# Performance work log

Hardware: AMD Instinct MI355X
Metric: run time of the kernel (lower is better)

The kernel has to match this reference:

```python
import jax, jax.numpy as jnp
import numpy as np

B = 8192          # tokens
H = 7168          # hidden size
E = 256           # routed experts
N_GROUP = 8
GROUP_SIZE = 32   # E // N_GROUP
TOPK_GROUP = 4
TOPK = 8
SCALE = 2.5
EPS = 1e-20
NEG_INF = -jnp.inf


def setup_inputs() -> dict:
    key = jax.random.key(0)
    k1, k2, k3 = jax.random.split(key, 3)
    x = jax.random.normal(k1, (1, 1, B, H), dtype=jnp.float32)
    weight = jax.random.normal(k2, (H, E), dtype=jnp.float32) * 0.02
    bias = jax.random.uniform(k3, (E,), dtype=jnp.float32)  # e_score_correction_bias
    return {"x": x, "weight": weight, "bias": bias}


def reference(x, weight, bias):
    # gate projection + softmax over experts
    logits = jnp.einsum('abth,he->abte', x, weight)          # [1,1,B,E]
    scores = jax.nn.softmax(logits, axis=-1)                 # [1,1,B,E]
    scores_with_bias = scores + bias                         # bias-corrected scores

    # group-limited routing: top-2 per group, summed -> group score
    grouped = scores_with_bias.reshape(1, 1, B, N_GROUP, GROUP_SIZE)
    top2_vals, _ = jax.lax.top_k(grouped, 2)                 # [1,1,B,8,2]
    group_scores = top2_vals.sum(axis=-1)                    # [1,1,B,8]

    # select top-4 groups, build {1, -inf} mask over groups
    _, top4_idx = jax.lax.top_k(group_scores, TOPK_GROUP)    # [1,1,B,4]
    sel = jax.nn.one_hot(top4_idx, N_GROUP, dtype=scores.dtype).sum(axis=-2)  # [1,1,B,8]
    group_mask = jnp.where(sel > 0, 1.0, NEG_INF)
    expert_mask = jnp.repeat(group_mask, GROUP_SIZE, axis=-1)  # [1,1,B,256]

    # mask (multiplicative, as in original), top-8 experts
    masked = scores_with_bias * expert_mask
    _, top8_idx = jax.lax.top_k(masked, TOPK)                # [1,1,B,8]

    # gather unbiased scores, normalize, eps + scale
    w = jnp.take_along_axis(scores, top8_idx, axis=-1)       # [1,1,B,8]
    w = w / w.sum(axis=-1, keepdims=True)
    w = (w + EPS) * SCALE
    return w, top8_idx
```

## Files before the change

kernel.cpp:

```cpp
#include <hip/hip_runtime.h>
#include <math.h>

#define B_TOK 8192
#define H_DIM 7168
#define E_NUM 256
#define NKS   8
#define KSL   (H_DIM / NKS)
#define BK    32
#define NSTEP (KSL / BK)
#define BM    128
#define NMT   (B_TOK / BM)
#define FLAG_CAP 512
#define TAU   2e-6

typedef _Float16 f16;
typedef __attribute__((ext_vector_type(8))) _Float16 f16x8;
typedef __attribute__((ext_vector_type(4))) float    f32x4;

typedef __attribute__((address_space(1))) const void gvoid_t;
typedef __attribute__((address_space(3))) void       lvoid_t;

__device__ inline void gload_lds16(const void* g, void* s) {
    __builtin_amdgcn_global_load_lds((gvoid_t*)g, (lvoid_t*)s, 16, 0, 0);
}

__device__ __forceinline__ void route_token(
    const double* lv, const double* bj, int l, int hf, int t,
    float* __restrict__ out, double* ming_adj, double* ming_grp)
{
    double m = fmax(fmax(lv[0], lv[1]), fmax(lv[2], lv[3]));
    #pragma unroll
    for (int d = 1; d < 64; d <<= 1) m = fmax(m, __shfl_xor(m, d, 64));
    double sc[4], zs = 0.0;
    #pragma unroll
    for (int q = 0; q < 4; ++q) { sc[q] = exp(lv[q] - m); zs += sc[q]; }
    #pragma unroll
    for (int d = 1; d < 64; d <<= 1) zs += __shfl_xor(zs, d, 64);
    double swb[4];
    #pragma unroll
    for (int q = 0; q < 4; ++q) { sc[q] /= zs; swb[q] = sc[q] + bj[q]; }

    double gsq[4];
    #pragma unroll
    for (int q = 0; q < 4; ++q) {
        double a = swb[q], b = -INFINITY;
        #pragma unroll
        for (int d = 1; d <= 16; d <<= 1) {
            double oa = __shfl_xor(a, d, 64), ob = __shfl_xor(b, d, 64);
            double na = fmax(a, oa);
            double nb = fmax(fmin(a, oa), fmax(b, ob));
            a = na; b = nb;
        }
        gsq[q] = a + b;
    }
    double gsv[8];
    #pragma unroll
    for (int q = 0; q < 4; ++q) {
        gsv[2 * q]     = __shfl(gsq[q], 0, 64);
        gsv[2 * q + 1] = __shfl(gsq[q], 32, 64);
    }

    unsigned selmask = 0; double g4 = 0.0, g5 = 0.0;
    #pragma unroll
    for (int k = 0; k < 5; ++k) {
        double best = -INFINITY; int bg = 0;
        #pragma unroll
        for (int g = 0; g < 8; ++g)
            if (gsv[g] > best) { best = gsv[g]; bg = g; }
        if (k < 4) { selmask |= 1u << bg; g4 = best; } else g5 = best;
        #pragma unroll
        for (int g = 0; g < 8; ++g) if (g == bg) gsv[g] = -INFINITY;
    }
    *ming_grp = g4 - g5;

    double mk[4];
    #pragma unroll
    for (int q = 0; q < 4; ++q)
        mk[q] = ((selmask >> (2 * q + hf)) & 1u) ? swb[q] : -INFINITY;

    double wk[8]; int ek[8]; double wsum = 0.0;
    double prev = 0.0, ming = 1e300;
    #pragma unroll
    for (int k = 0; k < 9; ++k) {
        double vbest = mk[0]; int ebest = l;
        #pragma unroll
        for (int q = 1; q < 4; ++q)
            if (mk[q] > vbest) { vbest = mk[q]; ebest = l + 64 * q; }
        #pragma unroll
        for (int d = 1; d < 64; d <<= 1) {
            double ov = __shfl_xor(vbest, d, 64);
            int    oe = __shfl_xor(ebest, d, 64);
            if (ov > vbest || (ov == vbest && oe < ebest)) { vbest = ov; ebest = oe; }
        }
        if (k > 0) ming = fmin(ming, prev - vbest);
        prev = vbest;
        if (k < 8) {
            const int ol = ebest & 63, oq = ebest >> 6;
            if (l == ol) {
                #pragma unroll
                for (int q = 0; q < 4; ++q) if (q == oq) mk[q] = -INFINITY;
            }
            double cand = (oq == 0) ? sc[0] : (oq == 1) ? sc[1] : (oq == 2) ? sc[2] : sc[3];
            double sv = __shfl(cand, ol, 64);
            wk[k] = sv; ek[k] = ebest; wsum += sv;
        }
    }
    *ming_adj = ming;

    if (l == 0) {
        const double inv = 1.0 / wsum;
        #pragma unroll
        for (int k = 0; k < 8; ++k) {
            out[(size_t)t * 8 + k] = (float)((wk[k] * inv + 1e-20) * 2.5);
            out[(size_t)B_TOK * 8 + (size_t)t * 8 + k] = (float)ek[k];
        }
    }
}

__global__ void convert_w_kernel(const float* __restrict__ W,
                                 f16* __restrict__ wpk,
                                 unsigned* __restrict__ flags) {
    if (blockIdx.x == 0 && threadIdx.x == 0) flags[0] = 0;
    int g = blockIdx.x * 256 + threadIdx.x;
    int n = g & 255, k = g >> 8;
    float v = W[(size_t)k * E_NUM + n];
    f16 hi = (f16)v;
    f16 lo = (f16)(v - (float)hi);
    int kf = k >> 5, tq = (k >> 3) & 3, j = k & 7;
    int nf = n >> 4, l = tq * 16 + (n & 15);
    size_t off = ((size_t)(kf * 32 + nf * 2)) * 512 + (size_t)l * 8 + j;
    wpk[off]       = hi;
    wpk[off + 512] = lo;
}

__device__ __forceinline__ void stage_B(const f16* __restrict__ wb, int kf,
                                        char* lds, int wid, int l) {
    #pragma unroll
    for (int i = 0; i < 4; ++i) {
        int fi = wid * 4 + i;
        gload_lds16(wb + ((size_t)kf * 32 + fi) * 512 + (size_t)l * 8,
                    lds + 16384 + fi * 1024);
    }
}

__device__ __forceinline__ void write_A(char* lds, int wid, int l,
                                        float4 a0, float4 a1) {
    float fv[8] = {a0.x, a0.y, a0.z, a0.w, a1.x, a1.y, a1.z, a1.w};
    f16x8 hv, lo;
    #pragma unroll
    for (int j = 0; j < 8; ++j) {
        f16 hh = (f16)fv[j];
        hv[j] = hh;
        lo[j] = (f16)(fv[j] - (float)hh);
    }
    *reinterpret_cast<f16x8*>(&lds[(wid * 2 + 0) * 1024 + l * 16]) = hv;
    *reinterpret_cast<f16x8*>(&lds[(wid * 2 + 1) * 1024 + l * 16]) = lo;
}

__device__ __forceinline__ void compute_step(const char* lds, int wr, int wc,
                                             int l, f32x4 (&acc)[4][4]) {
    const char* Ab = lds;
    const char* Bb = lds + 16384;
    f16x8 af[4][2], bf[4][2];
    #pragma unroll
    for (int mi = 0; mi < 4; ++mi)
        #pragma unroll
        for (int h = 0; h < 2; ++h)
            af[mi][h] = *reinterpret_cast<const f16x8*>(
                Ab + ((wr * 4 + mi) * 2 + h) * 1024 + l * 16);
    #pragma unroll
    for (int ni = 0; ni < 4; ++ni)
        #pragma unroll
        for (int h = 0; h < 2; ++h)
            bf[ni][h] = *reinterpret_cast<const f16x8*>(
                Bb + ((wc * 4 + ni) * 2 + h) * 1024 + l * 16);
    #pragma unroll
    for (int mi = 0; mi < 4; ++mi)
        #pragma unroll
        for (int ni = 0; ni < 4; ++ni) {
            acc[mi][ni] = __builtin_amdgcn_mfma_f32_16x16x32_f16(
                af[mi][0], bf[ni][0], acc[mi][ni], 0, 0, 0);
            acc[mi][ni] = __builtin_amdgcn_mfma_f32_16x16x32_f16(
                af[mi][0], bf[ni][1], acc[mi][ni], 0, 0, 0);
            acc[mi][ni] = __builtin_amdgcn_mfma_f32_16x16x32_f16(
                af[mi][1], bf[ni][0], acc[mi][ni], 0, 0, 0);
        }
}

__global__ __launch_bounds__(512, 4)
void gemm_kernel(const float* __restrict__ x,
                 const f16* __restrict__ wpk,
                 float* __restrict__ partial) {
    __shared__ __align__(16) char lds[49152];

    const int tid = threadIdx.x;
    const int l   = tid & 63;
    const int wid = tid >> 6;
    const int bid = blockIdx.x;
    const int ks  = bid & 7;
    const int mt  = bid >> 3;
    const int wr  = wid >> 2;
    const int wc  = wid & 3;

    const int row = mt * BM + wid * 16 + (l & 15);
    const float* xrow = x + (size_t)row * H_DIM + ks * KSL + (l >> 4) * 8;
    const f16* wb = wpk + (size_t)ks * NSTEP * 32 * 512;

    f32x4 acc[4][4];
    #pragma unroll
    for (int mi = 0; mi < 4; ++mi)
        #pragma unroll
        for (int ni = 0; ni < 4; ++ni) acc[mi][ni] = (f32x4)0.0f;

    float4 a0 = *reinterpret_cast<const float4*>(xrow);
    float4 a1 = *reinterpret_cast<const float4*>(xrow + 4);
    stage_B(wb, 0, lds, wid, l);
    write_A(lds, wid, l, a0, a1);
    a0 = *reinterpret_cast<const float4*>(xrow + BK);
    a1 = *reinterpret_cast<const float4*>(xrow + BK + 4);
    __syncthreads();

    for (int t = 0; t < NSTEP; ++t) {
        float4 a0n, a1n;
        if (t + 2 < NSTEP) {
            a0n = *reinterpret_cast<const float4*>(xrow + (size_t)(t + 2) * BK);
            a1n = *reinterpret_cast<const float4*>(xrow + (size_t)(t + 2) * BK + 4);
        }
        compute_step(lds, wr, wc, l, acc);
        __syncthreads();
        if (t + 1 < NSTEP) {
            stage_B(wb, t + 1, lds, wid, l);
            write_A(lds, wid, l, a0, a1);
            a0 = a0n; a1 = a1n;
            __syncthreads();
        }
    }

    float* pbase = partial + ((size_t)ks * B_TOK + (size_t)mt * BM) * E_NUM;
    #pragma unroll
    for (int mi = 0; mi < 4; ++mi)
        #pragma unroll
        for (int ni = 0; ni < 4; ++ni)
            #pragma unroll
            for (int r = 0; r < 4; ++r) {
                int rr = wr * 64 + mi * 16 + (l >> 4) * 4 + r;
                int cc = wc * 64 + ni * 16 + (l & 15);
                pbase[(size_t)rr * E_NUM + cc] = acc[mi][ni][r];
            }
}

__global__ __launch_bounds__(512, 1)
void routing_kernel(const float* __restrict__ partial,
                    const float* __restrict__ bias,
                    float* __restrict__ out,
                    unsigned* __restrict__ flags) {
    const int tid  = threadIdx.x;
    const int l    = tid & 63;
    const int wv   = tid >> 6;
    const int tok0 = blockIdx.x * 32;

    double bj[4];
    #pragma unroll
    for (int q = 0; q < 4; ++q) bj[q] = (double)bias[l + 64 * q];
    const int hf = l >> 5;

    for (int i = 0; i < 4; ++i) {
        const int t = tok0 + wv * 4 + i;
        double lv[4];
        #pragma unroll
        for (int q = 0; q < 4; ++q) {
            double s = 0.0;
            #pragma unroll
            for (int ksl = 0; ksl < NKS; ++ksl)
                s += (double)partial[((size_t)ksl * B_TOK + t) * E_NUM + l + 64 * q];
            lv[q] = s;
        }
        double ma, mg;
        route_token(lv, bj, l, hf, t, out, &ma, &mg);
        if (l == 0 && (ma < TAU || mg < TAU)) {
            unsigned idx = atomicAdd(&flags[0], 1u);
            if (idx < FLAG_CAP) flags[1 + idx] = (unsigned)t;
        }
    }
}

__global__ __launch_bounds__(256)
void recompute_dot_kernel(const float* __restrict__ x,
                          const float* __restrict__ W,
                          const unsigned* __restrict__ flags,
                          double* __restrict__ dpart) {
    __shared__ float xs[896];
    unsigned count = flags[0]; if (count > FLAG_CAP) count = FLAG_CAP;
    unsigned nj = count * 8;
    for (unsigned j = blockIdx.x; j < nj; j += gridDim.x) {
        unsigned li = j >> 3, sl = j & 7;
        int t = (int)flags[1 + li];
        const float* xb = x + (size_t)t * H_DIM + sl * 896;
        for (int i = threadIdx.x; i < 224; i += 256)
            *reinterpret_cast<float4*>(&xs[i * 4]) =
                *reinterpret_cast<const float4*>(xb + i * 4);
        __syncthreads();
        const float* wp = W + (size_t)(sl * 896) * E_NUM + threadIdx.x;
        double acc = 0.0;
        #pragma unroll 8
        for (int k = 0; k < 896; ++k)
            acc += (double)xs[k] * (double)wp[(size_t)k * E_NUM];
        dpart[((size_t)li * 8 + sl) * E_NUM + threadIdx.x] = acc;
        __syncthreads();
    }
}

__global__ __launch_bounds__(64)
void recompute_route_kernel(const double* __restrict__ dpart,
                            const float* __restrict__ bias,
                            const unsigned* __restrict__ flags,
                            float* __restrict__ out) {
    const int l = threadIdx.x;
    unsigned count = flags[0]; if (count > FLAG_CAP) count = FLAG_CAP;
    double bj[4];
    #pragma unroll
    for (int q = 0; q < 4; ++q) bj[q] = (double)bias[l + 64 * q];
    const int hf = l >> 5;
    for (unsigned li = blockIdx.x; li < count; li += gridDim.x) {
        int t = (int)flags[1 + li];
        double lv[4];
        #pragma unroll
        for (int q = 0; q < 4; ++q) {
            double s = 0.0;
            #pragma unroll
            for (int sl = 0; sl < 8; ++sl)
                s += dpart[((size_t)li * 8 + sl) * E_NUM + l + 64 * q];
            lv[q] = s;
        }
        double ma, mg;
        route_token(lv, bj, l, hf, t, out, &ma, &mg);
    }
}

#define TM 32
#define HB 64
#define FNST (H_DIM / HB)

__global__ __launch_bounds__(512, 1)
void moe_gate_fallback(const float* __restrict__ x,
                       const float* __restrict__ W,
                       const float* __restrict__ bias,
                       float* __restrict__ out) {
    __shared__ double xs[TM][HB];
    const int tid  = threadIdx.x;
    const int l    = tid & 63;
    const int wv   = tid >> 6;
    const int tok0 = blockIdx.x * TM;
    const int tl = tid >> 4;
    const int ho = (tid & 15) * 4;

    double acc[4][4];
    #pragma unroll
    for (int i = 0; i < 4; ++i)
        #pragma unroll
        for (int q = 0; q < 4; ++q) acc[i][q] = 0.0;

    const float* xrow = x + (size_t)(tok0 + tl) * H_DIM + ho;
    float4 v = *reinterpret_cast<const float4*>(xrow);

    for (int s = 0; s < FNST; ++s) {
        __syncthreads();
        xs[tl][ho + 0] = (double)v.x;
        xs[tl][ho + 1] = (double)v.y;
        xs[tl][ho + 2] = (double)v.z;
        xs[tl][ho + 3] = (double)v.w;
        __syncthreads();
        const int sn = (s + 1 < FNST) ? s + 1 : s;
        v = *reinterpret_cast<const float4*>(xrow + (size_t)sn * HB);
        const float* wh = W + (size_t)s * HB * E_NUM + l;
        #pragma unroll 4
        for (int h = 0; h < HB; h += 2) {
            float wf0[4], wf1[4];
            #pragma unroll
            for (int q = 0; q < 4; ++q) {
                wf0[q] = wh[(size_t)h       * E_NUM + q * 64];
                wf1[q] = wh[(size_t)(h + 1) * E_NUM + q * 64];
            }
            #pragma unroll
            for (int i = 0; i < 4; ++i) {
                const double2 xv = *reinterpret_cast<const double2*>(&xs[wv * 4 + i][h]);
                #pragma unroll
                for (int q = 0; q < 4; ++q) {
                    acc[i][q] = fma((double)wf0[q], xv.x, acc[i][q]);
                    acc[i][q] = fma((double)wf1[q], xv.y, acc[i][q]);
                }
            }
        }
    }

    double bj[4];
    #pragma unroll
    for (int q = 0; q < 4; ++q) bj[q] = (double)bias[l + 64 * q];
    const int hf = l >> 5;

    for (int i = 0; i < 4; ++i) {
        const int t = tok0 + wv * 4 + i;
        double lv[4];
        #pragma unroll
        for (int q = 0; q < 4; ++q) lv[q] = acc[i][q];
        double ma, mg;
        route_token(lv, bj, l, hf, t, out, &ma, &mg);
    }
}

extern "C" void kernel_launch(void* const* d_in, const int* in_sizes, int n_in,
                              void* d_out, int out_size, void* d_ws, size_t ws_size,
                              hipStream_t stream) {
    const float* x    = (const float*)d_in[0];
    const float* W    = (const float*)d_in[1];
    const float* bias = (const float*)d_in[2];
    float* out = (float*)d_out;

    const size_t flag_off = 7864320;
    const size_t part_off = 8u * 1024 * 1024;
    const size_t need     = part_off + (size_t)NKS * B_TOK * E_NUM * 4;

    if (ws_size >= need) {
        f16*      wpk     = (f16*)d_ws;
        unsigned* flags   = (unsigned*)((char*)d_ws + flag_off);
        float*    partial = (float*)((char*)d_ws + part_off);
        double*   dpart   = (double*)((char*)d_ws + part_off);

        convert_w_kernel<<<(H_DIM * E_NUM) / 256, 256, 0, stream>>>(W, wpk, flags);
        gemm_kernel<<<NMT * NKS, 512, 0, stream>>>(x, wpk, partial);
        routing_kernel<<<B_TOK / 32, 512, 0, stream>>>(partial, bias, out, flags);
        recompute_dot_kernel<<<1024, 256, 0, stream>>>(x, W, flags, dpart);
        recompute_route_kernel<<<64, 64, 0, stream>>>(dpart, bias, flags, out);
    } else {
        moe_gate_fallback<<<B_TOK / 32, 512, 0, stream>>>(x, W, bias, out);
    }
}
```

Baseline: 236.6 us.

## Retile GEMM to 64-row blocks, vectorize weight conversion, add MFMA priority

The GEMM tile drops from 128 to 64 rows, and blocks go from 512 to 256 threads. Each wave now covers all 64 rows and its own 64-column slice, which changes the A/B staging and LDS layout. The weight conversion kernel now has each thread write 8 packed halves as vector stores instead of scattered scalar stores. The MFMA loop is wrapped in s_setprio, and the recompute_dot launch size is halved. Together these target the conversion's store cost and GEMM occupancy and scheduling, at the cost of more redundant B loads per token.

New measurement: 231.0 us. -2.4%, faster.

```diff
diff --git a/kernel.cpp b/kernel.cpp
--- a/kernel.cpp
+++ b/kernel.cpp
@@ -8,7 +8,7 @@
 #define KSL   (H_DIM / NKS)
 #define BK    32
 #define NSTEP (KSL / BK)
-#define BM    128
+#define BM    64
 #define NMT   (B_TOK / BM)
 #define FLAG_CAP 512
 #define TAU   2e-6
@@ -121,30 +121,39 @@
                                  f16* __restrict__ wpk,
                                  unsigned* __restrict__ flags) {
     if (blockIdx.x == 0 && threadIdx.x == 0) flags[0] = 0;
-    int g = blockIdx.x * 256 + threadIdx.x;
-    int n = g & 255, k = g >> 8;
-    float v = W[(size_t)k * E_NUM + n];
-    f16 hi = (f16)v;
-    f16 lo = (f16)(v - (float)hi);
-    int kf = k >> 5, tq = (k >> 3) & 3, j = k & 7;
-    int nf = n >> 4, l = tq * 16 + (n & 15);
-    size_t off = ((size_t)(kf * 32 + nf * 2)) * 512 + (size_t)l * 8 + j;
-    wpk[off]       = hi;
-    wpk[off + 512] = lo;
+    int gid = blockIdx.x * 256 + threadIdx.x;
+    int fgp = gid >> 6;
+    int l   = gid & 63;
+    int kf = fgp >> 4, nf = fgp & 15;
+    int rb  = kf * 32 + (l >> 4) * 8;
+    int col = nf * 16 + (l & 15);
+    f16x8 hv, lv;
+    #pragma unroll
+    for (int j = 0; j < 8; ++j) {
+        float v = W[(size_t)(rb + j) * E_NUM + col];
+        f16 hh = (f16)v;
+        hv[j] = hh;
+        lv[j] = (f16)(v - (float)hh);
+    }
+    *reinterpret_cast<f16x8*>(&wpk[(size_t)fgp * 1024 + l * 8])       = hv;
+    *reinterpret_cast<f16x8*>(&wpk[(size_t)fgp * 1024 + 512 + l * 8]) = lv;
 }
 
 __device__ __forceinline__ void stage_B(const f16* __restrict__ wb, int kf,
                                         char* lds, int wid, int l) {
     #pragma unroll
-    for (int i = 0; i < 4; ++i) {
-        int fi = wid * 4 + i;
+    for (int i = 0; i < 8; ++i) {
+        int fi = wid * 8 + i;
         gload_lds16(wb + ((size_t)kf * 32 + fi) * 512 + (size_t)l * 8,
-                    lds + 16384 + fi * 1024);
-    }
-}
-
-__device__ __forceinline__ void write_A(char* lds, int wid, int l,
+                    lds + 8192 + fi * 1024);
+    }
+}
+
+__device__ __forceinline__ void write_A(char* lds, int tid,
                                         float4 a0, float4 a1) {
+    const int r  = tid >> 2;
+    const int mf = r >> 4;
+    const int l  = (tid & 3) * 16 + (r & 15);
     float fv[8] = {a0.x, a0.y, a0.z, a0.w, a1.x, a1.y, a1.z, a1.w};
     f16x8 hv, lo;
     #pragma unroll
@@ -153,27 +162,28 @@
         hv[j] = hh;
         lo[j] = (f16)(fv[j] - (float)hh);
     }
-    *reinterpret_cast<f16x8*>(&lds[(wid * 2 + 0) * 1024 + l * 16]) = hv;
-    *reinterpret_cast<f16x8*>(&lds[(wid * 2 + 1) * 1024 + l * 16]) = lo;
-}
-
-__device__ __forceinline__ void compute_step(const char* lds, int wr, int wc,
-                                             int l, f32x4 (&acc)[4][4]) {
+    *reinterpret_cast<f16x8*>(&lds[(mf * 2 + 0) * 1024 + l * 16]) = hv;
+    *reinterpret_cast<f16x8*>(&lds[(mf * 2 + 1) * 1024 + l * 16]) = lo;
+}
+
+__device__ __forceinline__ void compute_step(const char* lds, int wc, int l,
+                                             f32x4 (&acc)[4][4]) {
     const char* Ab = lds;
-    const char* Bb = lds + 16384;
+    const char* Bb = lds + 8192;
     f16x8 af[4][2], bf[4][2];
     #pragma unroll
     for (int mi = 0; mi < 4; ++mi)
         #pragma unroll
         for (int h = 0; h < 2; ++h)
             af[mi][h] = *reinterpret_cast<const f16x8*>(
-                Ab + ((wr * 4 + mi) * 2 + h) * 1024 + l * 16);
+                Ab + (mi * 2 + h) * 1024 + l * 16);
     #pragma unroll
     for (int ni = 0; ni < 4; ++ni)
         #pragma unroll
         for (int h = 0; h < 2; ++h)
             bf[ni][h] = *reinterpret_cast<const f16x8*>(
                 Bb + ((wc * 4 + ni) * 2 + h) * 1024 + l * 16);
+    __builtin_amdgcn_s_setprio(1);
     #pragma unroll
     for (int mi = 0; mi < 4; ++mi)
         #pragma unroll
@@ -185,13 +195,14 @@
             acc[mi][ni] = __builtin_amdgcn_mfma_f32_16x16x32_f16(
                 af[mi][1], bf[ni][0], acc[mi][ni], 0, 0, 0);
         }
-}
-
-__global__ __launch_bounds__(512, 4)
+    __builtin_amdgcn_s_setprio(0);
+}
+
+__global__ __launch_bounds__(256, 3)
 void gemm_kernel(const float* __restrict__ x,
                  const f16* __restrict__ wpk,
                  float* __restrict__ partial) {
-    __shared__ __align__(16) char lds[49152];
+    __shared__ __align__(16) char lds[40960];
 
     const int tid = threadIdx.x;
     const int l   = tid & 63;
@@ -199,11 +210,9 @@
     const int bid = blockIdx.x;
     const int ks  = bid & 7;
     const int mt  = bid >> 3;
-    const int wr  = wid >> 2;
-    const int wc  = wid & 3;
-
-    const int row = mt * BM + wid * 16 + (l & 15);
-    const float* xrow = x + (size_t)row * H_DIM + ks * KSL + (l >> 4) * 8;
+
+    const float* xrow = x + (size_t)(mt * BM + (tid >> 2)) * H_DIM
+                          + ks * KSL + (tid & 3) * 8;
     const f16* wb = wpk + (size_t)ks * NSTEP * 32 * 512;
 
     f32x4 acc[4][4];
@@ -215,7 +224,7 @@
     float4 a0 = *reinterpret_cast<const float4*>(xrow);
     float4 a1 = *reinterpret_cast<const float4*>(xrow + 4);
     stage_B(wb, 0, lds, wid, l);
-    write_A(lds, wid, l, a0, a1);
+    write_A(lds, tid, a0, a1);
     a0 = *reinterpret_cast<const float4*>(xrow + BK);
     a1 = *reinterpret_cast<const float4*>(xrow + BK + 4);
     __syncthreads();
@@ -226,11 +235,11 @@
             a0n = *reinterpret_cast<const float4*>(xrow + (size_t)(t + 2) * BK);
             a1n = *reinterpret_cast<const float4*>(xrow + (size_t)(t + 2) * BK + 4);
         }
-        compute_step(lds, wr, wc, l, acc);
+        compute_step(lds, wid, l, acc);
         __syncthreads();
         if (t + 1 < NSTEP) {
             stage_B(wb, t + 1, lds, wid, l);
-            write_A(lds, wid, l, a0, a1);
+            write_A(lds, tid, a0, a1);
             a0 = a0n; a1 = a1n;
             __syncthreads();
         }
@@ -243,8 +252,8 @@
         for (int ni = 0; ni < 4; ++ni)
             #pragma unroll
             for (int r = 0; r < 4; ++r) {
-                int rr = wr * 64 + mi * 16 + (l >> 4) * 4 + r;
-                int cc = wc * 64 + ni * 16 + (l & 15);
+                int rr = mi * 16 + (l >> 4) * 4 + r;
+                int cc = wid * 64 + ni * 16 + (l & 15);
                 pbase[(size_t)rr * E_NUM + cc] = acc[mi][ni][r];
             }
 }
@@ -426,10 +435,10 @@
         float*    partial = (float*)((char*)d_ws + part_off);
         double*   dpart   = (double*)((char*)d_ws + part_off);
 
-        convert_w_kernel<<<(H_DIM * E_NUM) / 256, 256, 0, stream>>>(W, wpk, flags);
-        gemm_kernel<<<NMT * NKS, 512, 0, stream>>>(x, wpk, partial);
+        convert_w_kernel<<<896, 256, 0, stream>>>(W, wpk, flags);
+        gemm_kernel<<<NMT * NKS, 256, 0, stream>>>(x, wpk, partial);
         routing_kernel<<<B_TOK / 32, 512, 0, stream>>>(partial, bias, out, flags);
-        recompute_dot_kernel<<<1024, 256, 0, stream>>>(x, W, flags, dpart);
+        recompute_dot_kernel<<<512, 256, 0, stream>>>(x, W, flags, dpart);
         recompute_route_kernel<<<64, 64, 0, stream>>>(dpart, bias, flags, out);
     } else {
         moe_gate_fallback<<<B_TOK / 32, 512, 0, stream>>>(x, W, bias, out);
```
